# Kernel optimization log

Hardware: AMD Instinct MI355X
Metric: run time of the kernel (lower is better)

The kernel has to match this reference:

```python
import jax, jax.numpy as jnp
import numpy as np

RATIO = 4   # compression ratio (group size)
H = 6       # index heads
D = 64      # index head dim = max(8, 768//6//2)
TOPK = 8    # index_topk
EPS = 1e-6  # rms_norm eps


def rms_norm(x):
    return x * jax.lax.rsqrt(jnp.mean(jnp.square(x), axis=-1, keepdims=True) + EPS)


def setup_inputs() -> dict:
    key = jax.random.key(0)
    k1, k2, k3, k4, k5 = jax.random.split(key, 5)
    B, T, E = 4, 4096, 768
    s = 0.02
    return {
        "x": jax.random.normal(k1, (B, T, E), jnp.float32),
        "wq": jax.random.normal(k2, (E, H * D), jnp.float32) * s,
        "wk": jax.random.normal(k3, (E, H * D), jnp.float32) * s,
        "wg": jax.random.normal(k4, (E, H * D), jnp.float32) * s,
        "ape": jax.random.normal(k5, (RATIO, H, D), jnp.float32) * s,
    }


def reference(x, wq, wk, wg, ape):
    B, T, E = x.shape
    G = -(-T // RATIO)          # ceil(T / ratio)
    pad = G * RATIO - T

    # --- compress keys: gated pooling over ratio-groups ---
    k = (x @ wk).reshape(B, T, H, D)
    gate = (x @ wg).reshape(B, T, H, D)
    if pad:
        k = jnp.pad(k, ((0, 0), (0, pad), (0, 0), (0, 0)))
        gate = jnp.pad(gate, ((0, 0), (0, pad), (0, 0), (0, 0)), constant_values=-jnp.inf)
    k = k.reshape(B, G, RATIO, H, D)
    gate = gate.reshape(B, G, RATIO, H, D) + ape[None, None]
    w = jax.nn.softmax(gate.astype(jnp.float32), axis=2).astype(k.dtype)
    keys = rms_norm(jnp.sum(k * w, axis=2))           # [B,G,H,D]
    group_ends = jnp.minimum(jnp.arange(RATIO - 1, G * RATIO, RATIO), T - 1)  # [G]

    # --- query-key scores ---
    q = rms_norm((x @ wq).reshape(B, T, H, D))
    scores = jnp.einsum('bthd,bghd->bhtg', q, keys) * (D ** -0.5)
    scores = jnp.mean(scores, axis=1)                 # [B,T,G]

    # --- causal mask over group ends, then top-k selection ---
    causal = group_ends[None, None, :] <= jnp.arange(T)[None, :, None]  # [1,T,G]
    scores = jnp.where(causal, scores, -jnp.inf)
    topk = min(TOPK, G)
    _, sel = jax.lax.top_k(scores, topk)              # [B,T,topk]

    # scatter selected indices into boolean mask
    bi = jnp.arange(B)[:, None, None]
    ti = jnp.arange(T)[None, :, None]
    mask = jnp.zeros((B, T, G), dtype=bool).at[bi, ti, sel].set(True)
    return (mask & causal, group_ends)
```

## Files before the change

### kernel.cpp

```cpp
#include <hip/hip_runtime.h>
#include <hip/hip_bf16.h>
#include <math.h>

#define B_    4
#define T_    4096
#define E_    768
#define H_    6
#define D_    64
#define HD_   384
#define G_    1024
#define RATIO_ 4
#define TOPK_ 8
#define MT_   (B_*T_)
#define NS_   1152

typedef __attribute__((ext_vector_type(8))) short short8;
typedef __attribute__((ext_vector_type(4))) float f32x4;
typedef __hip_bfloat16 bf16;

#define GLD16(g, l) __builtin_amdgcn_global_load_lds( \
    (const __attribute__((address_space(1))) void*)(g), \
    (__attribute__((address_space(3))) void*)(l), 16, 0, 0)

static __device__ __forceinline__ unsigned short f2bf(float f) {
  bf16 h = __float2bfloat16(f);
  return __builtin_bit_cast(unsigned short, h);
}
static __device__ __forceinline__ unsigned umax_(unsigned a, unsigned b) { return a > b ? a : b; }
static __device__ __forceinline__ unsigned umin_(unsigned a, unsigned b) { return a > b ? b : a; }

__global__ __launch_bounds__(256) void cvt_x_kernel(
    const float* __restrict__ in, bf16* __restrict__ out)
{
  size_t i = (size_t)blockIdx.x * 256 + threadIdx.x;
  const float4* p = reinterpret_cast<const float4*>(in) + i * 2;
  float4 v0 = p[0], v1 = p[1];
  float f[8] = {v0.x, v0.y, v0.z, v0.w, v1.x, v1.y, v1.z, v1.w};
  union { unsigned short u[8]; short8 v; } r;
#pragma unroll
  for (int k = 0; k < 8; ++k) r.u[k] = f2bf(f[k]);
  *reinterpret_cast<short8*>(out + i * 8) = r.v;
}

__global__ __launch_bounds__(256) void cvt_w_t(
    const float* __restrict__ wq, const float* __restrict__ wk,
    const float* __restrict__ wg, bf16* __restrict__ outbase)
{
  const int z = blockIdx.z;
  const float* src = z == 0 ? wq : (z == 1 ? wk : wg);
  __shared__ float t[32][33];
  int r = threadIdx.x >> 5, c = threadIdx.x & 31;
  int k0 = blockIdx.x * 32, n0 = blockIdx.y * 32;
#pragma unroll
  for (int i = 0; i < 4; ++i)
    t[r + i * 8][c] = src[(size_t)(k0 + r + i * 8) * HD_ + n0 + c];
  __syncthreads();
#pragma unroll
  for (int i = 0; i < 4; ++i) {
    int cc = n0 + r + i * 8;
    int ro = (z == 0) ? cc : 384 + ((cc >> 4) << 5) + ((z - 1) << 4) + (cc & 15);
    outbase[(size_t)ro * E_ + k0 + c] = __float2bfloat16(t[c][r + i * 8]);
  }
}

__global__ __launch_bounds__(256, 3) void gemm_qkg_mfma(
    const bf16* __restrict__ X, const bf16* __restrict__ Ws,
    const float* __restrict__ ape, bf16* __restrict__ Q,
    bf16* __restrict__ keys)
{
  __shared__ bf16 lds[3][4096];
  const int tid = threadIdx.x;
  const int lane = tid & 63, wv = tid >> 6;
  const int ll = lane & 15, lh = lane >> 4;
  const int m0 = blockIdx.x * 128, n0 = blockIdx.y * 128;
  const int srow = tid >> 2;
  const int scol = (((tid & 3) ^ ((tid >> 3) & 3)) << 3);
  const bf16* pB0 = Ws + (size_t)(n0 + srow) * E_ + scol;
  const bf16* pB1 = Ws + (size_t)(n0 + 64 + srow) * E_ + scol;
  const bf16* pA0 = X + (size_t)(m0 + wv * 32 + ll) * E_ + lh * 8;
  const bf16* pA1 = pA0 + (size_t)16 * E_;

#define STAGE(b, k0) do { \
    char* base_ = (char*)&lds[b][0] + tid * 16; \
    GLD16(pB0 + (k0), base_); \
    GLD16(pB1 + (k0), base_ + 4096); \
  } while (0)

  f32x4 acc[2][8];
#pragma unroll
  for (int m = 0; m < 2; ++m)
#pragma unroll
    for (int n = 0; n < 8; ++n) acc[m][n] = (f32x4){0.f, 0.f, 0.f, 0.f};
  const int asw = (lh ^ ((ll >> 1) & 3)) << 3;

  short8 curA0 = *reinterpret_cast<const short8*>(pA0);
  short8 curA1 = *reinterpret_cast<const short8*>(pA1);
  STAGE(0, 0);
  STAGE(1, 32);
  short8 nxtA0 = curA0, nxtA1 = curA1;

#pragma unroll
  for (int k = 0; k < 24; ++k) {
    const int k0 = k * 32;
    if (k < 23) {
      nxtA0 = *reinterpret_cast<const short8*>(pA0 + k0 + 32);
      nxtA1 = *reinterpret_cast<const short8*>(pA1 + k0 + 32);
    }
    if (k < 22) STAGE((k + 2) % 3, k0 + 64);
    if (k < 22)       asm volatile("s_waitcnt vmcnt(6)" ::: "memory");
    else if (k == 22) asm volatile("s_waitcnt vmcnt(4)" ::: "memory");
    else              asm volatile("s_waitcnt vmcnt(0)" ::: "memory");
    __builtin_amdgcn_s_barrier();
    __builtin_amdgcn_sched_barrier(0);
    const bf16* Lb = &lds[k % 3][0];
    short8 b[8];
#pragma unroll
    for (int n = 0; n < 8; ++n)
      b[n] = *reinterpret_cast<const short8*>(&Lb[(n * 16 + ll) * 32 + asw]);
    asm volatile("s_waitcnt lgkmcnt(0)" ::: "memory");
    __builtin_amdgcn_sched_barrier(0);
    __builtin_amdgcn_s_barrier();
#pragma unroll
    for (int m = 0; m < 2; ++m) {
      short8 am = (m == 0) ? curA0 : curA1;
#pragma unroll
      for (int n = 0; n < 8; ++n)
        acc[m][n] = __builtin_amdgcn_mfma_f32_16x16x32_bf16(am, b[n], acc[m][n], 0, 0, 0);
    }
    curA0 = nxtA0; curA1 = nxtA1;
  }
#undef STAGE

  if (blockIdx.y < 3) {
#pragma unroll
    for (int m = 0; m < 2; ++m)
#pragma unroll
      for (int j = 0; j < 4; ++j) {
        int row = m0 + wv * 32 + m * 16 + lh * 4 + j;
#pragma unroll
        for (int h = 0; h < 2; ++h) {
          float ss = 0.f;
#pragma unroll
          for (int n = 4 * h; n < 4 * h + 4; ++n) ss += acc[m][n][j] * acc[m][n][j];
          ss += __shfl_xor(ss, 1, 64); ss += __shfl_xor(ss, 2, 64);
          ss += __shfl_xor(ss, 4, 64); ss += __shfl_xor(ss, 8, 64);
          float scl = rsqrtf(ss * (1.0f / D_) + 1e-6f);
#pragma unroll
          for (int n = 4 * h; n < 4 * h + 4; ++n)
            Q[(size_t)row * HD_ + n0 + n * 16 + ll] =
                __float2bfloat16(acc[m][n][j] * scl);
        }
      }
  } else {
    const int hcb = (n0 - 384) >> 1;
    float apev[4][4];
#pragma unroll
    for (int p = 0; p < 4; ++p) {
      int hc = hcb + p * 16 + ll;
#pragma unroll
      for (int j = 0; j < 4; ++j) apev[p][j] = ape[j * HD_ + hc];
    }
#pragma unroll
    for (int m = 0; m < 2; ++m) {
      float pooled[4];
#pragma unroll
      for (int p = 0; p < 4; ++p) {
        float g0 = acc[m][2 * p + 1][0] + apev[p][0];
        float g1 = acc[m][2 * p + 1][1] + apev[p][1];
        float g2 = acc[m][2 * p + 1][2] + apev[p][2];
        float g3 = acc[m][2 * p + 1][3] + apev[p][3];
        float mx = fmaxf(fmaxf(g0, g1), fmaxf(g2, g3));
        float e0 = expf(g0 - mx), e1 = expf(g1 - mx);
        float e2 = expf(g2 - mx), e3 = expf(g3 - mx);
        float inv = 1.0f / (e0 + e1 + e2 + e3);
        pooled[p] = (acc[m][2 * p][0] * e0 + acc[m][2 * p][1] * e1 +
                     acc[m][2 * p][2] * e2 + acc[m][2 * p][3] * e3) * inv;
      }
      float ss = pooled[0] * pooled[0] + pooled[1] * pooled[1] +
                 pooled[2] * pooled[2] + pooled[3] * pooled[3];
      ss += __shfl_xor(ss, 1, 64); ss += __shfl_xor(ss, 2, 64);
      ss += __shfl_xor(ss, 4, 64); ss += __shfl_xor(ss, 8, 64);
      float scl = rsqrtf(ss * (1.0f / D_) + 1e-6f);
      int prow = (m0 >> 2) + wv * 8 + m * 4 + lh;
#pragma unroll
      for (int p = 0; p < 4; ++p)
        keys[(size_t)prow * HD_ + hcb + p * 16 + ll] =
            __float2bfloat16(pooled[p] * scl);
    }
  }
}

__global__ __launch_bounds__(256, 4) void score_topk_fused(
    const bf16* __restrict__ Qall, const bf16* __restrict__ Kall,
    int* __restrict__ mask, int* __restrict__ ends)
{
  const int x = blockIdx.x;
  const int b = blockIdx.y;
  const int s = (b < 2) ? x : 255 - x;
  const int t0 = s << 4;
  const int tid = threadIdx.x;
  const int w = tid >> 6;
  const int lane = tid & 63;
  const int ll = lane & 15, lh = lane >> 4;

  __shared__ unsigned top[4][16][8];

  if (x == 0 && b == 0) {
    int g = tid;
#pragma unroll
    for (int c = 0; c < 4; ++c, g += 256) {
      int e = (g << 2) + 3;
      ends[g] = e < T_ - 1 ? e : T_ - 1;
    }
  }

  int* mbase = mask + ((size_t)b * T_ + t0) * G_;
  {
    int4* m4 = reinterpret_cast<int4*>(mbase);
    const int4 z = make_int4(0, 0, 0, 0);
#pragma unroll
    for (int i = 0; i < 16; ++i) m4[i * 256 + tid] = z;
  }

  const bf16* Qb = Qall + (size_t)b * T_ * HD_;
  const bf16* Kb = Kall + (size_t)b * G_ * HD_;
  const int t = t0 + ll;
  const int gmax = (t + 1) >> 2;
  const int nmega = ((t0 >> 2) + 4 + 63) >> 6;

  short8 qf[12];
  {
    const bf16* pQ = Qb + (size_t)t * HD_ + lh * 8;
#pragma unroll
    for (int k = 0; k < 12; ++k)
      qf[k] = *reinterpret_cast<const short8*>(pQ + k * 32);
  }

  unsigned v0 = 0, v1 = 0, v2 = 0, v3 = 0, v4 = 0, v5 = 0, v6 = 0, v7 = 0;
#define INS(xx) do { unsigned k_ = (xx), t_; \
    t_ = umax_(v0, k_); k_ = umin_(v0, k_); v0 = t_; \
    t_ = umax_(v1, k_); k_ = umin_(v1, k_); v1 = t_; \
    t_ = umax_(v2, k_); k_ = umin_(v2, k_); v2 = t_; \
    t_ = umax_(v3, k_); k_ = umin_(v3, k_); v3 = t_; \
    t_ = umax_(v4, k_); k_ = umin_(v4, k_); v4 = t_; \
    t_ = umax_(v5, k_); k_ = umin_(v5, k_); v5 = t_; \
    t_ = umax_(v6, k_); k_ = umin_(v6, k_); v6 = t_; \
    t_ = umax_(v7, k_); k_ = umin_(v7, k_); v7 = t_; } while (0)

  for (int mg = w; mg < nmega; mg += 4) {
    const int g0 = mg << 6;
    const bf16* pK = Kb + (size_t)(g0 + ll) * HD_ + lh * 8;
    short8 kf[12][4];
#pragma unroll
    for (int kk = 0; kk < 12; ++kk)
#pragma unroll
      for (int tl = 0; tl < 4; ++tl)
        kf[kk][tl] = *reinterpret_cast<const short8*>(
            pK + (size_t)tl * 16 * HD_ + kk * 32);
    f32x4 acc[4];
#pragma unroll
    for (int tl = 0; tl < 4; ++tl) acc[tl] = (f32x4){0.f, 0.f, 0.f, 0.f};
#pragma unroll
    for (int kk = 0; kk < 12; ++kk)
#pragma unroll
      for (int tl = 0; tl < 4; ++tl)
        acc[tl] = __builtin_amdgcn_mfma_f32_16x16x32_bf16(
            kf[kk][tl], qf[kk], acc[tl], 0, 0, 0);
#pragma unroll
    for (int tl = 0; tl < 4; ++tl)
#pragma unroll
      for (int j = 0; j < 4; ++j) {
        int g = g0 + tl * 16 + lh * 4 + j;
        float xv = acc[tl][j] + 512.0f;
        unsigned key = (g < gmax)
            ? ((__builtin_bit_cast(unsigned, xv) & 0xFFFFFC00u) |
               (unsigned)(1023 - g))
            : 0u;
        INS(key);
      }
  }
#undef INS

#define CEx(a, bb) { unsigned h_ = umax_(a, bb), l_ = umin_(a, bb); a = h_; bb = l_; }
#define MERGE4() \
  _Pragma("unroll") \
  for (int st = 0; st < 2; ++st) { \
    const int off = 16 << st; \
    unsigned p0 = (unsigned)__shfl_xor((int)v0, off, 64); \
    unsigned p1 = (unsigned)__shfl_xor((int)v1, off, 64); \
    unsigned p2 = (unsigned)__shfl_xor((int)v2, off, 64); \
    unsigned p3 = (unsigned)__shfl_xor((int)v3, off, 64); \
    unsigned p4 = (unsigned)__shfl_xor((int)v4, off, 64); \
    unsigned p5 = (unsigned)__shfl_xor((int)v5, off, 64); \
    unsigned p6 = (unsigned)__shfl_xor((int)v6, off, 64); \
    unsigned p7 = (unsigned)__shfl_xor((int)v7, off, 64); \
    unsigned w0 = umax_(v0, p7), w1 = umax_(v1, p6); \
    unsigned w2 = umax_(v2, p5), w3 = umax_(v3, p4); \
    unsigned w4 = umax_(v4, p3), w5 = umax_(v5, p2); \
    unsigned w6 = umax_(v6, p1), w7 = umax_(v7, p0); \
    CEx(w0, w4); CEx(w1, w5); CEx(w2, w6); CEx(w3, w7); \
    CEx(w0, w2); CEx(w1, w3); CEx(w4, w6); CEx(w5, w7); \
    CEx(w0, w1); CEx(w2, w3); CEx(w4, w5); CEx(w6, w7); \
    v0 = w0; v1 = w1; v2 = w2; v3 = w3; v4 = w4; v5 = w5; v6 = w6; v7 = w7; \
  }

  MERGE4();

  if (lh == 0) {
    unsigned* tp = &top[w][ll][0];
    tp[0] = v0; tp[1] = v1; tp[2] = v2; tp[3] = v3;
    tp[4] = v4; tp[5] = v5; tp[6] = v6; tp[7] = v7;
  }
  __syncthreads();

  if (w == 0) {
    const unsigned* tp = &top[lh][ll][0];
    v0 = tp[0]; v1 = tp[1]; v2 = tp[2]; v3 = tp[3];
    v4 = tp[4]; v5 = tp[5]; v6 = tp[6]; v7 = tp[7];
    MERGE4();
    if (lh == 0) {
      int* rb = mbase + (size_t)ll * G_;
      if (v0) rb[1023 - (v0 & 1023)] = 1;
      if (v1) rb[1023 - (v1 & 1023)] = 1;
      if (v2) rb[1023 - (v2 & 1023)] = 1;
      if (v3) rb[1023 - (v3 & 1023)] = 1;
      if (v4) rb[1023 - (v4 & 1023)] = 1;
      if (v5) rb[1023 - (v5 & 1023)] = 1;
      if (v6) rb[1023 - (v6 & 1023)] = 1;
      if (v7) rb[1023 - (v7 & 1023)] = 1;
    }
  }
#undef MERGE4
#undef CEx
}

extern "C" void kernel_launch(void* const* d_in, const int* in_sizes, int n_in,
                              void* d_out, int out_size, void* d_ws, size_t ws_size,
                              hipStream_t stream)
{
  const float* x   = (const float*)d_in[0];
  const float* wq  = (const float*)d_in[1];
  const float* wk  = (const float*)d_in[2];
  const float* wg  = (const float*)d_in[3];
  const float* ape = (const float*)d_in[4];

  bf16* Ws   = (bf16*)d_ws;
  bf16* qb   = Ws + (size_t)NS_ * E_;
  bf16* keys = qb + (size_t)MT_ * HD_;

  bf16* xb = (bf16*)d_out;

  cvt_x_kernel<<<dim3(MT_ * E_ / 8 / 256), dim3(256), 0, stream>>>(x, xb);
  cvt_w_t<<<dim3(E_ / 32, HD_ / 32, 3), dim3(256), 0, stream>>>(wq, wk, wg, Ws);

  gemm_qkg_mfma<<<dim3(MT_ / 128, NS_ / 128), dim3(256), 0, stream>>>(
      xb, Ws, ape, qb, keys);

  score_topk_fused<<<dim3(256, B_), dim3(256), 0, stream>>>(
      qb, keys, (int*)d_out, (int*)d_out + (size_t)B_ * T_ * G_);
}
```

Before: 121.0 us.

## Widen score/topk block to 8 waves, stage Q in LDS, batch top-k insertion

Measured after the change: 134.5 us. 1.11x slower.

```diff
diff --git a/kernel.cpp b/kernel.cpp
--- a/kernel.cpp
+++ b/kernel.cpp
@@ -190,7 +190,7 @@
   }
 }
 
-__global__ __launch_bounds__(256, 4) void score_topk_fused(
+__global__ __launch_bounds__(512, 8) void score_topk_fused(
     const bf16* __restrict__ Qall, const bf16* __restrict__ Kall,
     int* __restrict__ mask, int* __restrict__ ends)
 {
@@ -203,12 +203,13 @@
   const int lane = tid & 63;
   const int ll = lane & 15, lh = lane >> 4;
 
-  __shared__ unsigned top[4][16][8];
+  __shared__ short qls[16 * 384];
+  __shared__ unsigned top[8][16][8];
 
   if (x == 0 && b == 0) {
     int g = tid;
 #pragma unroll
-    for (int c = 0; c < 4; ++c, g += 256) {
+    for (int c = 0; c < 2; ++c, g += 512) {
       int e = (g << 2) + 3;
       ends[g] = e < T_ - 1 ? e : T_ - 1;
     }
@@ -219,7 +220,7 @@
     int4* m4 = reinterpret_cast<int4*>(mbase);
     const int4 z = make_int4(0, 0, 0, 0);
 #pragma unroll
-    for (int i = 0; i < 16; ++i) m4[i * 256 + tid] = z;
+    for (int i = 0; i < 8; ++i) m4[i * 512 + tid] = z;
   }
 
   const bf16* Qb = Qall + (size_t)b * T_ * HD_;
@@ -228,60 +229,83 @@
   const int gmax = (t + 1) >> 2;
   const int nmega = ((t0 >> 2) + 4 + 63) >> 6;
 
-  short8 qf[12];
   {
-    const bf16* pQ = Qb + (size_t)t * HD_ + lh * 8;
-#pragma unroll
-    for (int k = 0; k < 12; ++k)
-      qf[k] = *reinterpret_cast<const short8*>(pQ + k * 32);
-  }
+    int r = tid / 48, sc = tid % 48;
+    short8 qv = *reinterpret_cast<const short8*>(
+        Qb + (size_t)(t0 + r) * HD_ + sc * 8);
+    *reinterpret_cast<short8*>(&qls[r * 384 + ((sc ^ (r & 7)) << 3)]) = qv;
+    if (tid < 256) {
+      int c1 = tid + 512;
+      int r1 = c1 / 48, s1 = c1 % 48;
+      short8 qv1 = *reinterpret_cast<const short8*>(
+          Qb + (size_t)(t0 + r1) * HD_ + s1 * 8);
+      *reinterpret_cast<short8*>(&qls[r1 * 384 + ((s1 ^ (r1 & 7)) << 3)]) = qv1;
+    }
+  }
+  __syncthreads();
 
   unsigned v0 = 0, v1 = 0, v2 = 0, v3 = 0, v4 = 0, v5 = 0, v6 = 0, v7 = 0;
-#define INS(xx) do { unsigned k_ = (xx), t_; \
-    t_ = umax_(v0, k_); k_ = umin_(v0, k_); v0 = t_; \
-    t_ = umax_(v1, k_); k_ = umin_(v1, k_); v1 = t_; \
-    t_ = umax_(v2, k_); k_ = umin_(v2, k_); v2 = t_; \
-    t_ = umax_(v3, k_); k_ = umin_(v3, k_); v3 = t_; \
-    t_ = umax_(v4, k_); k_ = umin_(v4, k_); v4 = t_; \
-    t_ = umax_(v5, k_); k_ = umin_(v5, k_); v5 = t_; \
-    t_ = umax_(v6, k_); k_ = umin_(v6, k_); v6 = t_; \
-    t_ = umax_(v7, k_); k_ = umin_(v7, k_); v7 = t_; } while (0)
-
-  for (int mg = w; mg < nmega; mg += 4) {
+
+#define CEx(a, bb) { unsigned h_ = umax_(a, bb), l_ = umin_(a, bb); a = h_; bb = l_; }
+#define SORT8(A, o) do { \
+    CEx(A[o+0],A[o+1]); CEx(A[o+2],A[o+3]); CEx(A[o+4],A[o+5]); CEx(A[o+6],A[o+7]); \
+    CEx(A[o+0],A[o+2]); CEx(A[o+1],A[o+3]); CEx(A[o+4],A[o+6]); CEx(A[o+5],A[o+7]); \
+    CEx(A[o+1],A[o+2]); CEx(A[o+5],A[o+6]); \
+    CEx(A[o+0],A[o+4]); CEx(A[o+1],A[o+5]); CEx(A[o+2],A[o+6]); CEx(A[o+3],A[o+7]); \
+    CEx(A[o+2],A[o+4]); CEx(A[o+3],A[o+5]); \
+    CEx(A[o+1],A[o+2]); CEx(A[o+3],A[o+4]); CEx(A[o+5],A[o+6]); \
+  } while (0)
+#define CLEAN8(E) do { \
+    CEx(E[0],E[4]); CEx(E[1],E[5]); CEx(E[2],E[6]); CEx(E[3],E[7]); \
+    CEx(E[0],E[2]); CEx(E[1],E[3]); CEx(E[4],E[6]); CEx(E[5],E[7]); \
+    CEx(E[0],E[1]); CEx(E[2],E[3]); CEx(E[4],E[5]); CEx(E[6],E[7]); \
+  } while (0)
+
+  for (int mg = w; mg < nmega; mg += 8) {
     const int g0 = mg << 6;
     const bf16* pK = Kb + (size_t)(g0 + ll) * HD_ + lh * 8;
-    short8 kf[12][4];
-#pragma unroll
-    for (int kk = 0; kk < 12; ++kk)
-#pragma unroll
-      for (int tl = 0; tl < 4; ++tl)
-        kf[kk][tl] = *reinterpret_cast<const short8*>(
+    f32x4 acc[4];
+#pragma unroll
+    for (int tl = 0; tl < 4; ++tl) acc[tl] = (f32x4){0.f, 0.f, 0.f, 0.f};
+#pragma unroll
+    for (int kk = 0; kk < 12; ++kk) {
+      short8 qf = *reinterpret_cast<const short8*>(
+          &qls[ll * 384 + (((lh + kk * 4) ^ (ll & 7)) << 3)]);
+#pragma unroll
+      for (int tl = 0; tl < 4; ++tl) {
+        short8 kf = *reinterpret_cast<const short8*>(
             pK + (size_t)tl * 16 * HD_ + kk * 32);
-    f32x4 acc[4];
-#pragma unroll
-    for (int tl = 0; tl < 4; ++tl) acc[tl] = (f32x4){0.f, 0.f, 0.f, 0.f};
-#pragma unroll
-    for (int kk = 0; kk < 12; ++kk)
-#pragma unroll
-      for (int tl = 0; tl < 4; ++tl)
-        acc[tl] = __builtin_amdgcn_mfma_f32_16x16x32_bf16(
-            kf[kk][tl], qf[kk], acc[tl], 0, 0, 0);
+        acc[tl] = __builtin_amdgcn_mfma_f32_16x16x32_bf16(kf, qf, acc[tl], 0, 0, 0);
+      }
+    }
+    unsigned c[16];
 #pragma unroll
     for (int tl = 0; tl < 4; ++tl)
 #pragma unroll
       for (int j = 0; j < 4; ++j) {
         int g = g0 + tl * 16 + lh * 4 + j;
         float xv = acc[tl][j] + 512.0f;
-        unsigned key = (g < gmax)
+        c[tl * 4 + j] = (g < gmax)
             ? ((__builtin_bit_cast(unsigned, xv) & 0xFFFFFC00u) |
                (unsigned)(1023 - g))
             : 0u;
-        INS(key);
       }
-  }
-#undef INS
-
-#define CEx(a, bb) { unsigned h_ = umax_(a, bb), l_ = umin_(a, bb); a = h_; bb = l_; }
+    SORT8(c, 0);
+    SORT8(c, 8);
+    unsigned e[8];
+#pragma unroll
+    for (int i = 0; i < 8; ++i) e[i] = umax_(c[i], c[15 - i]);
+    CLEAN8(e);
+    unsigned nv[8];
+    nv[0] = umax_(v0, e[7]); nv[1] = umax_(v1, e[6]);
+    nv[2] = umax_(v2, e[5]); nv[3] = umax_(v3, e[4]);
+    nv[4] = umax_(v4, e[3]); nv[5] = umax_(v5, e[2]);
+    nv[6] = umax_(v6, e[1]); nv[7] = umax_(v7, e[0]);
+    CLEAN8(nv);
+    v0 = nv[0]; v1 = nv[1]; v2 = nv[2]; v3 = nv[3];
+    v4 = nv[4]; v5 = nv[5]; v6 = nv[6]; v7 = nv[7];
+  }
+
 #define MERGE4() \
   _Pragma("unroll") \
   for (int st = 0; st < 2; ++st) { \
@@ -313,11 +337,41 @@
   }
   __syncthreads();
 
-  if (w == 0) {
-    const unsigned* tp = &top[lh][ll][0];
+  if (w < 2) {
+    const unsigned* tp = &top[w * 4 + lh][ll][0];
     v0 = tp[0]; v1 = tp[1]; v2 = tp[2]; v3 = tp[3];
     v4 = tp[4]; v5 = tp[5]; v6 = tp[6]; v7 = tp[7];
     MERGE4();
+    if (lh == 0) {
+      unsigned* dp = &top[w * 4][ll][0];
+      dp[0] = v0; dp[1] = v1; dp[2] = v2; dp[3] = v3;
+      dp[4] = v4; dp[5] = v5; dp[6] = v6; dp[7] = v7;
+    }
+  }
+  __syncthreads();
+
+  if (w == 0) {
+    const unsigned* tp = &top[(lh & 1) * 4][ll][0];
+    v0 = tp[0]; v1 = tp[1]; v2 = tp[2]; v3 = tp[3];
+    v4 = tp[4]; v5 = tp[5]; v6 = tp[6]; v7 = tp[7];
+    {
+      unsigned p0 = (unsigned)__shfl_xor((int)v0, 16, 64);
+      unsigned p1 = (unsigned)__shfl_xor((int)v1, 16, 64);
+      unsigned p2 = (unsigned)__shfl_xor((int)v2, 16, 64);
+      unsigned p3 = (unsigned)__shfl_xor((int)v3, 16, 64);
+      unsigned p4 = (unsigned)__shfl_xor((int)v4, 16, 64);
+      unsigned p5 = (unsigned)__shfl_xor((int)v5, 16, 64);
+      unsigned p6 = (unsigned)__shfl_xor((int)v6, 16, 64);
+      unsigned p7 = (unsigned)__shfl_xor((int)v7, 16, 64);
+      unsigned w0 = umax_(v0, p7), w1 = umax_(v1, p6);
+      unsigned w2 = umax_(v2, p5), w3 = umax_(v3, p4);
+      unsigned w4 = umax_(v4, p3), w5 = umax_(v5, p2);
+      unsigned w6 = umax_(v6, p1), w7 = umax_(v7, p0);
+      CEx(w0, w4); CEx(w1, w5); CEx(w2, w6); CEx(w3, w7);
+      CEx(w0, w2); CEx(w1, w3); CEx(w4, w6); CEx(w5, w7);
+      CEx(w0, w1); CEx(w2, w3); CEx(w4, w5); CEx(w6, w7);
+      v0 = w0; v1 = w1; v2 = w2; v3 = w3; v4 = w4; v5 = w5; v6 = w6; v7 = w7;
+    }
     if (lh == 0) {
       int* rb = mbase + (size_t)ll * G_;
       if (v0) rb[1023 - (v0 & 1023)] = 1;
@@ -331,6 +385,8 @@
     }
   }
 #undef MERGE4
+#undef CLEAN8
+#undef SORT8
 #undef CEx
 }
 
@@ -356,6 +412,6 @@
   gemm_qkg_mfma<<<dim3(MT_ / 128, NS_ / 128), dim3(256), 0, stream>>>(
       xb, Ws, ape, qb, keys);
 
-  score_topk_fused<<<dim3(256, B_), dim3(256), 0, stream>>>(
+  score_topk_fused<<<dim3(256, B_), dim3(512), 0, stream>>>(
       qb, keys, (int*)d_out, (int*)d_out + (size_t)B_ * T_ * G_);
 }
```

## Use 2x2 wave tiling in QKG GEMM and bitonic-network top-k insertion

Applied to the files above, without the earlier changes.

New measurement: 148.4 us. 22.7% more time.

```diff
diff --git a/kernel.cpp b/kernel.cpp
--- a/kernel.cpp
+++ b/kernel.cpp
@@ -63,22 +63,26 @@
   }
 }
 
-__global__ __launch_bounds__(256, 3) void gemm_qkg_mfma(
+__global__ __launch_bounds__(256, 2) void gemm_qkg_mfma(
     const bf16* __restrict__ X, const bf16* __restrict__ Ws,
     const float* __restrict__ ape, bf16* __restrict__ Q,
     bf16* __restrict__ keys)
 {
   __shared__ bf16 lds[3][4096];
+  __shared__ float ssx[2][2][4][4];
   const int tid = threadIdx.x;
   const int lane = tid & 63, wv = tid >> 6;
+  const int wm = wv >> 1, wn = wv & 1;
   const int ll = lane & 15, lh = lane >> 4;
   const int m0 = blockIdx.x * 128, n0 = blockIdx.y * 128;
   const int srow = tid >> 2;
   const int scol = (((tid & 3) ^ ((tid >> 3) & 3)) << 3);
   const bf16* pB0 = Ws + (size_t)(n0 + srow) * E_ + scol;
   const bf16* pB1 = Ws + (size_t)(n0 + 64 + srow) * E_ + scol;
-  const bf16* pA0 = X + (size_t)(m0 + wv * 32 + ll) * E_ + lh * 8;
-  const bf16* pA1 = pA0 + (size_t)16 * E_;
+  const bf16* pA[4];
+#pragma unroll
+  for (int r = 0; r < 4; ++r)
+    pA[r] = X + (size_t)(m0 + wm * 64 + r * 16 + ll) * E_ + lh * 8;
 
 #define STAGE(b, k0) do { \
     char* base_ = (char*)&lds[b][0] + tid * 16; \
@@ -86,85 +90,85 @@
     GLD16(pB1 + (k0), base_ + 4096); \
   } while (0)
 
-  f32x4 acc[2][8];
-#pragma unroll
-  for (int m = 0; m < 2; ++m)
-#pragma unroll
-    for (int n = 0; n < 8; ++n) acc[m][n] = (f32x4){0.f, 0.f, 0.f, 0.f};
+  f32x4 acc[4][4];
+#pragma unroll
+  for (int m = 0; m < 4; ++m)
+#pragma unroll
+    for (int n = 0; n < 4; ++n) acc[m][n] = (f32x4){0.f, 0.f, 0.f, 0.f};
   const int asw = (lh ^ ((ll >> 1) & 3)) << 3;
 
-  short8 curA0 = *reinterpret_cast<const short8*>(pA0);
-  short8 curA1 = *reinterpret_cast<const short8*>(pA1);
+  short8 curA[4], nxtA[4];
+#pragma unroll
+  for (int r = 0; r < 4; ++r) curA[r] = *reinterpret_cast<const short8*>(pA[r]);
   STAGE(0, 0);
   STAGE(1, 32);
-  short8 nxtA0 = curA0, nxtA1 = curA1;
+#pragma unroll
+  for (int r = 0; r < 4; ++r) nxtA[r] = curA[r];
 
 #pragma unroll
   for (int k = 0; k < 24; ++k) {
     const int k0 = k * 32;
     if (k < 23) {
-      nxtA0 = *reinterpret_cast<const short8*>(pA0 + k0 + 32);
-      nxtA1 = *reinterpret_cast<const short8*>(pA1 + k0 + 32);
+#pragma unroll
+      for (int r = 0; r < 4; ++r)
+        nxtA[r] = *reinterpret_cast<const short8*>(pA[r] + k0 + 32);
     }
     if (k < 22) STAGE((k + 2) % 3, k0 + 64);
-    if (k < 22)       asm volatile("s_waitcnt vmcnt(6)" ::: "memory");
-    else if (k == 22) asm volatile("s_waitcnt vmcnt(4)" ::: "memory");
+    if (k < 22)       asm volatile("s_waitcnt vmcnt(8)" ::: "memory");
+    else if (k == 22) asm volatile("s_waitcnt vmcnt(6)" ::: "memory");
     else              asm volatile("s_waitcnt vmcnt(0)" ::: "memory");
     __builtin_amdgcn_s_barrier();
     __builtin_amdgcn_sched_barrier(0);
     const bf16* Lb = &lds[k % 3][0];
-    short8 b[8];
-#pragma unroll
-    for (int n = 0; n < 8; ++n)
-      b[n] = *reinterpret_cast<const short8*>(&Lb[(n * 16 + ll) * 32 + asw]);
+    short8 b[4];
+#pragma unroll
+    for (int n = 0; n < 4; ++n)
+      b[n] = *reinterpret_cast<const short8*>(
+          &Lb[(wn * 64 + n * 16 + ll) * 32 + asw]);
     asm volatile("s_waitcnt lgkmcnt(0)" ::: "memory");
     __builtin_amdgcn_sched_barrier(0);
     __builtin_amdgcn_s_barrier();
 #pragma unroll
-    for (int m = 0; m < 2; ++m) {
-      short8 am = (m == 0) ? curA0 : curA1;
-#pragma unroll
-      for (int n = 0; n < 8; ++n)
-        acc[m][n] = __builtin_amdgcn_mfma_f32_16x16x32_bf16(am, b[n], acc[m][n], 0, 0, 0);
-    }
-    curA0 = nxtA0; curA1 = nxtA1;
+    for (int m = 0; m < 4; ++m)
+#pragma unroll
+      for (int n = 0; n < 4; ++n)
+        acc[m][n] = __builtin_amdgcn_mfma_f32_16x16x32_bf16(curA[m], b[n], acc[m][n], 0, 0, 0);
+#pragma unroll
+    for (int r = 0; r < 4; ++r) curA[r] = nxtA[r];
   }
 #undef STAGE
 
   if (blockIdx.y < 3) {
 #pragma unroll
-    for (int m = 0; m < 2; ++m)
+    for (int m = 0; m < 4; ++m)
 #pragma unroll
       for (int j = 0; j < 4; ++j) {
-        int row = m0 + wv * 32 + m * 16 + lh * 4 + j;
-#pragma unroll
-        for (int h = 0; h < 2; ++h) {
-          float ss = 0.f;
-#pragma unroll
-          for (int n = 4 * h; n < 4 * h + 4; ++n) ss += acc[m][n][j] * acc[m][n][j];
-          ss += __shfl_xor(ss, 1, 64); ss += __shfl_xor(ss, 2, 64);
-          ss += __shfl_xor(ss, 4, 64); ss += __shfl_xor(ss, 8, 64);
-          float scl = rsqrtf(ss * (1.0f / D_) + 1e-6f);
-#pragma unroll
-          for (int n = 4 * h; n < 4 * h + 4; ++n)
-            Q[(size_t)row * HD_ + n0 + n * 16 + ll] =
-                __float2bfloat16(acc[m][n][j] * scl);
-        }
+        float ss = 0.f;
+#pragma unroll
+        for (int n = 0; n < 4; ++n) ss += acc[m][n][j] * acc[m][n][j];
+        ss += __shfl_xor(ss, 1, 64); ss += __shfl_xor(ss, 2, 64);
+        ss += __shfl_xor(ss, 4, 64); ss += __shfl_xor(ss, 8, 64);
+        float scl = rsqrtf(ss * (1.0f / D_) + 1e-6f);
+        int row = m0 + wm * 64 + m * 16 + lh * 4 + j;
+#pragma unroll
+        for (int n = 0; n < 4; ++n)
+          Q[(size_t)row * HD_ + n0 + wn * 64 + n * 16 + ll] =
+              __float2bfloat16(acc[m][n][j] * scl);
       }
   } else {
     const int hcb = (n0 - 384) >> 1;
-    float apev[4][4];
-#pragma unroll
-    for (int p = 0; p < 4; ++p) {
-      int hc = hcb + p * 16 + ll;
+    float apev[2][4];
+#pragma unroll
+    for (int p = 0; p < 2; ++p) {
+      int hc = hcb + (wn * 2 + p) * 16 + ll;
 #pragma unroll
       for (int j = 0; j < 4; ++j) apev[p][j] = ape[j * HD_ + hc];
     }
-#pragma unroll
-    for (int m = 0; m < 2; ++m) {
-      float pooled[4];
-#pragma unroll
-      for (int p = 0; p < 4; ++p) {
+    float pooled[4][2];
+#pragma unroll
+    for (int m = 0; m < 4; ++m) {
+#pragma unroll
+      for (int p = 0; p < 2; ++p) {
         float g0 = acc[m][2 * p + 1][0] + apev[p][0];
         float g1 = acc[m][2 * p + 1][1] + apev[p][1];
         float g2 = acc[m][2 * p + 1][2] + apev[p][2];
@@ -173,19 +177,24 @@
         float e0 = expf(g0 - mx), e1 = expf(g1 - mx);
         float e2 = expf(g2 - mx), e3 = expf(g3 - mx);
         float inv = 1.0f / (e0 + e1 + e2 + e3);
-        pooled[p] = (acc[m][2 * p][0] * e0 + acc[m][2 * p][1] * e1 +
-                     acc[m][2 * p][2] * e2 + acc[m][2 * p][3] * e3) * inv;
+        pooled[m][p] = (acc[m][2 * p][0] * e0 + acc[m][2 * p][1] * e1 +
+                        acc[m][2 * p][2] * e2 + acc[m][2 * p][3] * e3) * inv;
       }
-      float ss = pooled[0] * pooled[0] + pooled[1] * pooled[1] +
-                 pooled[2] * pooled[2] + pooled[3] * pooled[3];
+      float ss = pooled[m][0] * pooled[m][0] + pooled[m][1] * pooled[m][1];
       ss += __shfl_xor(ss, 1, 64); ss += __shfl_xor(ss, 2, 64);
       ss += __shfl_xor(ss, 4, 64); ss += __shfl_xor(ss, 8, 64);
+      if (ll == 0) ssx[wm][wn][m][lh] = ss;
+    }
+    __syncthreads();
+#pragma unroll
+    for (int m = 0; m < 4; ++m) {
+      float ss = ssx[wm][0][m][lh] + ssx[wm][1][m][lh];
       float scl = rsqrtf(ss * (1.0f / D_) + 1e-6f);
-      int prow = (m0 >> 2) + wv * 8 + m * 4 + lh;
-#pragma unroll
-      for (int p = 0; p < 4; ++p)
-        keys[(size_t)prow * HD_ + hcb + p * 16 + ll] =
-            __float2bfloat16(pooled[p] * scl);
+      int prow = (m0 >> 2) + wm * 16 + m * 4 + lh;
+#pragma unroll
+      for (int p = 0; p < 2; ++p)
+        keys[(size_t)prow * HD_ + hcb + (wn * 2 + p) * 16 + ll] =
+            __float2bfloat16(pooled[m][p] * scl);
     }
   }
 }
@@ -237,15 +246,21 @@
   }
 
   unsigned v0 = 0, v1 = 0, v2 = 0, v3 = 0, v4 = 0, v5 = 0, v6 = 0, v7 = 0;
-#define INS(xx) do { unsigned k_ = (xx), t_; \
-    t_ = umax_(v0, k_); k_ = umin_(v0, k_); v0 = t_; \
-    t_ = umax_(v1, k_); k_ = umin_(v1, k_); v1 = t_; \
-    t_ = umax_(v2, k_); k_ = umin_(v2, k_); v2 = t_; \
-    t_ = umax_(v3, k_); k_ = umin_(v3, k_); v3 = t_; \
-    t_ = umax_(v4, k_); k_ = umin_(v4, k_); v4 = t_; \
-    t_ = umax_(v5, k_); k_ = umin_(v5, k_); v5 = t_; \
-    t_ = umax_(v6, k_); k_ = umin_(v6, k_); v6 = t_; \
-    t_ = umax_(v7, k_); k_ = umin_(v7, k_); v7 = t_; } while (0)
+
+#define CEx(a, bb) { unsigned h_ = umax_(a, bb), l_ = umin_(a, bb); a = h_; bb = l_; }
+#define SORT8(A, o) do { \
+    CEx(A[o+0],A[o+1]); CEx(A[o+2],A[o+3]); CEx(A[o+4],A[o+5]); CEx(A[o+6],A[o+7]); \
+    CEx(A[o+0],A[o+2]); CEx(A[o+1],A[o+3]); CEx(A[o+4],A[o+6]); CEx(A[o+5],A[o+7]); \
+    CEx(A[o+1],A[o+2]); CEx(A[o+5],A[o+6]); \
+    CEx(A[o+0],A[o+4]); CEx(A[o+1],A[o+5]); CEx(A[o+2],A[o+6]); CEx(A[o+3],A[o+7]); \
+    CEx(A[o+2],A[o+4]); CEx(A[o+3],A[o+5]); \
+    CEx(A[o+1],A[o+2]); CEx(A[o+3],A[o+4]); CEx(A[o+5],A[o+6]); \
+  } while (0)
+#define CLEAN8(E) do { \
+    CEx(E[0],E[4]); CEx(E[1],E[5]); CEx(E[2],E[6]); CEx(E[3],E[7]); \
+    CEx(E[0],E[2]); CEx(E[1],E[3]); CEx(E[4],E[6]); CEx(E[5],E[7]); \
+    CEx(E[0],E[1]); CEx(E[2],E[3]); CEx(E[4],E[5]); CEx(E[6],E[7]); \
+  } while (0)
 
   for (int mg = w; mg < nmega; mg += 4) {
     const int g0 = mg << 6;
@@ -266,22 +281,34 @@
       for (int tl = 0; tl < 4; ++tl)
         acc[tl] = __builtin_amdgcn_mfma_f32_16x16x32_bf16(
             kf[kk][tl], qf[kk], acc[tl], 0, 0, 0);
+    unsigned c[16];
 #pragma unroll
     for (int tl = 0; tl < 4; ++tl)
 #pragma unroll
       for (int j = 0; j < 4; ++j) {
         int g = g0 + tl * 16 + lh * 4 + j;
         float xv = acc[tl][j] + 512.0f;
-        unsigned key = (g < gmax)
+        c[tl * 4 + j] = (g < gmax)
             ? ((__builtin_bit_cast(unsigned, xv) & 0xFFFFFC00u) |
                (unsigned)(1023 - g))
             : 0u;
-        INS(key);
       }
-  }
-#undef INS
-
-#define CEx(a, bb) { unsigned h_ = umax_(a, bb), l_ = umin_(a, bb); a = h_; bb = l_; }
+    SORT8(c, 0);
+    SORT8(c, 8);
+    unsigned e[8];
+#pragma unroll
+    for (int i = 0; i < 8; ++i) e[i] = umax_(c[i], c[15 - i]);
+    CLEAN8(e);
+    unsigned nv[8];
+    nv[0] = umax_(v0, e[7]); nv[1] = umax_(v1, e[6]);
+    nv[2] = umax_(v2, e[5]); nv[3] = umax_(v3, e[4]);
+    nv[4] = umax_(v4, e[3]); nv[5] = umax_(v5, e[2]);
+    nv[6] = umax_(v6, e[1]); nv[7] = umax_(v7, e[0]);
+    CLEAN8(nv);
+    v0 = nv[0]; v1 = nv[1]; v2 = nv[2]; v3 = nv[3];
+    v4 = nv[4]; v5 = nv[5]; v6 = nv[6]; v7 = nv[7];
+  }
+
 #define MERGE4() \
   _Pragma("unroll") \
   for (int st = 0; st < 2; ++st) { \
@@ -331,6 +358,8 @@
     }
   }
 #undef MERGE4
+#undef CLEAN8
+#undef SORT8
 #undef CEx
 }
 
```

## Restructure QKG GEMM mainloop to 64-wide K steps with double buffering

Applied to the files above, without the earlier changes.

Result: no change. 120.3 us (-0.5%).

```diff
diff --git a/kernel.cpp b/kernel.cpp
--- a/kernel.cpp
+++ b/kernel.cpp
@@ -68,68 +68,89 @@
     const float* __restrict__ ape, bf16* __restrict__ Q,
     bf16* __restrict__ keys)
 {
-  __shared__ bf16 lds[3][4096];
+  __shared__ bf16 lds[2][8192];
   const int tid = threadIdx.x;
   const int lane = tid & 63, wv = tid >> 6;
   const int ll = lane & 15, lh = lane >> 4;
   const int m0 = blockIdx.x * 128, n0 = blockIdx.y * 128;
-  const int srow = tid >> 2;
-  const int scol = (((tid & 3) ^ ((tid >> 3) & 3)) << 3);
-  const bf16* pB0 = Ws + (size_t)(n0 + srow) * E_ + scol;
-  const bf16* pB1 = Ws + (size_t)(n0 + 64 + srow) * E_ + scol;
+  const int srow = tid >> 3;
+  const int sslot = (((tid & 7) ^ ((tid >> 3) & 7)) << 3);
+  const bf16* pS = Ws + (size_t)(n0 + srow) * E_ + sslot;
   const bf16* pA0 = X + (size_t)(m0 + wv * 32 + ll) * E_ + lh * 8;
   const bf16* pA1 = pA0 + (size_t)16 * E_;
 
 #define STAGE(b, k0) do { \
     char* base_ = (char*)&lds[b][0] + tid * 16; \
-    GLD16(pB0 + (k0), base_); \
-    GLD16(pB1 + (k0), base_ + 4096); \
+    GLD16(pS + (k0),            base_); \
+    GLD16(pS + 32 * E_ + (k0),  base_ + 4096); \
+    GLD16(pS + 64 * E_ + (k0),  base_ + 8192); \
+    GLD16(pS + 96 * E_ + (k0),  base_ + 12288); \
   } while (0)
+#define LOAD_A(dst, k0) do { \
+    dst[0][0] = *reinterpret_cast<const short8*>(pA0 + (k0)); \
+    dst[0][1] = *reinterpret_cast<const short8*>(pA0 + (k0) + 32); \
+    dst[1][0] = *reinterpret_cast<const short8*>(pA1 + (k0)); \
+    dst[1][1] = *reinterpret_cast<const short8*>(pA1 + (k0) + 32); \
+  } while (0)
 
   f32x4 acc[2][8];
 #pragma unroll
   for (int m = 0; m < 2; ++m)
 #pragma unroll
     for (int n = 0; n < 8; ++n) acc[m][n] = (f32x4){0.f, 0.f, 0.f, 0.f};
-  const int asw = (lh ^ ((ll >> 1) & 3)) << 3;
-
-  short8 curA0 = *reinterpret_cast<const short8*>(pA0);
-  short8 curA1 = *reinterpret_cast<const short8*>(pA1);
+
+  short8 curA[2][2], nxtA[2][2];
+  LOAD_A(curA, 0);
   STAGE(0, 0);
-  STAGE(1, 32);
-  short8 nxtA0 = curA0, nxtA1 = curA1;
-
-#pragma unroll
-  for (int k = 0; k < 24; ++k) {
-    const int k0 = k * 32;
-    if (k < 23) {
-      nxtA0 = *reinterpret_cast<const short8*>(pA0 + k0 + 32);
-      nxtA1 = *reinterpret_cast<const short8*>(pA1 + k0 + 32);
-    }
-    if (k < 22) STAGE((k + 2) % 3, k0 + 64);
-    if (k < 22)       asm volatile("s_waitcnt vmcnt(6)" ::: "memory");
-    else if (k == 22) asm volatile("s_waitcnt vmcnt(4)" ::: "memory");
-    else              asm volatile("s_waitcnt vmcnt(0)" ::: "memory");
+#pragma unroll
+  for (int m = 0; m < 2; ++m)
+#pragma unroll
+    for (int s = 0; s < 2; ++s) nxtA[m][s] = curA[m][s];
+
+#pragma unroll
+  for (int k = 0; k < 12; ++k) {
+    const int k0 = k * 64;
+    if (k < 11) {
+      LOAD_A(nxtA, k0 + 64);
+      STAGE((k + 1) & 1, k0 + 64);
+    }
+    if (k < 11) asm volatile("s_waitcnt vmcnt(8)" ::: "memory");
+    else        asm volatile("s_waitcnt vmcnt(0)" ::: "memory");
     __builtin_amdgcn_s_barrier();
     __builtin_amdgcn_sched_barrier(0);
-    const bf16* Lb = &lds[k % 3][0];
-    short8 b[8];
+    const bf16* Lb = &lds[k & 1][0];
+    short8 b0[8];
 #pragma unroll
     for (int n = 0; n < 8; ++n)
-      b[n] = *reinterpret_cast<const short8*>(&Lb[(n * 16 + ll) * 32 + asw]);
+      b0[n] = *reinterpret_cast<const short8*>(
+          &Lb[(n * 16 + ll) * 64 + ((lh ^ (ll & 7)) << 3)]);
+    asm volatile("s_waitcnt lgkmcnt(0)" ::: "memory");
+    __builtin_amdgcn_sched_barrier(0);
+#pragma unroll
+    for (int m = 0; m < 2; ++m)
+#pragma unroll
+      for (int n = 0; n < 8; ++n)
+        acc[m][n] = __builtin_amdgcn_mfma_f32_16x16x32_bf16(curA[m][0], b0[n], acc[m][n], 0, 0, 0);
+    short8 b1[8];
+#pragma unroll
+    for (int n = 0; n < 8; ++n)
+      b1[n] = *reinterpret_cast<const short8*>(
+          &Lb[(n * 16 + ll) * 64 + (((4 + lh) ^ (ll & 7)) << 3)]);
     asm volatile("s_waitcnt lgkmcnt(0)" ::: "memory");
     __builtin_amdgcn_sched_barrier(0);
     __builtin_amdgcn_s_barrier();
 #pragma unroll
-    for (int m = 0; m < 2; ++m) {
-      short8 am = (m == 0) ? curA0 : curA1;
+    for (int m = 0; m < 2; ++m)
 #pragma unroll
       for (int n = 0; n < 8; ++n)
-        acc[m][n] = __builtin_amdgcn_mfma_f32_16x16x32_bf16(am, b[n], acc[m][n], 0, 0, 0);
-    }
-    curA0 = nxtA0; curA1 = nxtA1;
+        acc[m][n] = __builtin_amdgcn_mfma_f32_16x16x32_bf16(curA[m][1], b1[n], acc[m][n], 0, 0, 0);
+#pragma unroll
+    for (int m = 0; m < 2; ++m)
+#pragma unroll
+      for (int s = 0; s < 2; ++s) curA[m][s] = nxtA[m][s];
   }
 #undef STAGE
+#undef LOAD_A
 
   if (blockIdx.y < 3) {
 #pragma unroll
```
